# Kernel optimization log

Measured on AMD Instinct MI355X. Metric: run time of the kernel, lower is better.

## Reference

```python
import jax, jax.numpy as jnp
import numpy as np
from jax import lax

DIM = 192
HID = DIM // 2  # ffn_expansion_factor = 0.5 hardcoded in CFIM
B, H, W = 8, 160, 160
LAMBDA_C = 0.5
LAMBDA_S = 0.5


def _dwconv(x, w, dil):
    # depthwise 3x3 conv, NCHW, weight (C,1,3,3), 'same' padding with dilation
    return lax.conv_general_dilated(
        x, w, window_strides=(1, 1), padding=((dil, dil), (dil, dil)),
        rhs_dilation=(dil, dil), feature_group_count=w.shape[0],
        dimension_numbers=('NCHW', 'OIHW', 'NCHW'))


def setup_inputs() -> dict:
    key = jax.random.key(0)
    ks = jax.random.split(key, 12)
    s = 0.02
    return {
        'x1': jax.random.normal(ks[0], (B, DIM, H, W), jnp.float32),
        'x2': jax.random.normal(ks[1], (B, DIM, H, W), jnp.float32),
        # ChannelWeights MLP (reduction=1): Linear(4d,4d) -> ReLU -> Linear(4d,2d) -> Sigmoid
        'mlp_w1': jax.random.normal(ks[2], (4 * DIM, 4 * DIM), jnp.float32) * s,
        'mlp_b1': jnp.zeros((4 * DIM,), jnp.float32),
        'mlp_w2': jax.random.normal(ks[3], (2 * DIM, 4 * DIM), jnp.float32) * s,
        'mlp_b2': jnp.zeros((2 * DIM,), jnp.float32),
        # SpatialWeights: pointwise project_in (no bias), 3 depthwise 3x3, pointwise project_out
        'w_in': jax.random.normal(ks[4], (3 * HID, 2 * DIM), jnp.float32) * s,
        'w_dw1': jax.random.normal(ks[5], (HID, 1, 3, 3), jnp.float32) * s,  # center depth slice of the (3,3,3) kernel; padded-zero depth slices contribute nothing
        'w_dw2': jax.random.normal(ks[6], (HID, 1, 3, 3), jnp.float32) * s,
        'w_dw3': jax.random.normal(ks[7], (HID, 1, 3, 3), jnp.float32) * s,
        'w_out': jax.random.normal(ks[8], (2 * DIM, HID), jnp.float32) * s,
    }


def reference(x1, x2, mlp_w1, mlp_b1, mlp_w2, mlp_b2,
              w_in, w_dw1, w_dw2, w_dw3, w_out):
    b = x1.shape[0]
    dim = x1.shape[1]
    x = jnp.concatenate([x1, x2], axis=1)  # (B, 2*dim, H, W)

    # --- ChannelWeights ---
    avg = jnp.mean(x, axis=(2, 3))          # (B, 2*dim)
    mx = jnp.max(x, axis=(2, 3))            # (B, 2*dim)
    y = jnp.concatenate([avg, mx], axis=1)  # (B, 4*dim)
    y = jax.nn.relu(y @ mlp_w1.T + mlp_b1)
    y = jax.nn.sigmoid(y @ mlp_w2.T + mlp_b2)  # (B, 2*dim)
    cw = y.reshape(b, 2, dim, 1, 1)
    cw0, cw1 = cw[:, 0], cw[:, 1]           # each (B, dim, 1, 1)

    # --- SpatialWeights ---
    p = jnp.einsum('bchw,oc->bohw', x, w_in)  # 1x1 'Conv3d' project_in
    a, g2, g3 = jnp.split(p, 3, axis=1)       # each (B, HID, H, W)
    a = _dwconv(a, w_dw1, 1)
    g2 = _dwconv(g2, w_dw2, 2)
    g3 = _dwconv(g3, w_dw3, 3)
    g = jax.nn.gelu(a, approximate=False) * (g2 + g3)
    sw = jnp.einsum('bchw,oc->bohw', g, w_out)  # (B, 2*dim, H, W)
    sw0, sw1 = jnp.split(sw, 2, axis=1)

    # --- combine ---
    out_x1 = x1 + LAMBDA_C * cw1 * x2 + LAMBDA_S * sw1
    out_x2 = x2 + LAMBDA_C * cw0 * x1 + LAMBDA_S * sw0
    return (out_x1, out_x2)
```

## Files before the change

kernel.cpp:

```cpp
#include <hip/hip_runtime.h>
#include <cstdint>

#define HW 25600
#define WIDTH 160
#define NB 8
#define DIM 192
#define CH2 384
#define PCH 288
#define HID 96
#define PROW 176
#define PPS 29216
#define OUTN 39321600

typedef short bf16x8 __attribute__((ext_vector_type(8)));
typedef float f32x4 __attribute__((ext_vector_type(4)));

__device__ __forceinline__ unsigned short f2bf(float f) {
  union { float f; unsigned int u; } v; v.f = f;
  unsigned int u = v.u;
  u += 0x7FFFu + ((u >> 16) & 1u);
  return (unsigned short)(u >> 16);
}
__device__ __forceinline__ float bf2f(unsigned int bits16) {
  union { unsigned int u; float f; } v; v.u = bits16 << 16;
  return v.f;
}

__global__ void k_prep(const float* __restrict__ w, unsigned short* __restrict__ wa) {
  int i = blockIdx.x * 256 + threadIdx.x;
  float4 v = *(const float4*)(w + (size_t)i * 4);
  unsigned int lo = (unsigned int)f2bf(v.x) | ((unsigned int)f2bf(v.y) << 16);
  unsigned int hi = (unsigned int)f2bf(v.z) | ((unsigned int)f2bf(v.w) << 16);
  *(uint2*)(wa + (size_t)i * 4) = make_uint2(lo, hi);
}

__global__ void k_padzero(unsigned short* __restrict__ p) {
  unsigned short* base = p + (size_t)blockIdx.x * PPS;
  for (int i = threadIdx.x; i < 3616; i += 256) {
    int row, col;
    if (i < 1056) {
      int r = i / PROW; col = i - r * PROW;
      row = (r < 3) ? r : 160 + r;
    } else {
      int j = i - 1056;
      int r = j >> 4, cc = j & 15;
      row = 3 + r;
      col = (cc < 8) ? cc : 160 + cc;
    }
    base[row * PROW + col] = 0;
  }
}

__global__ void k_mlp1(const float* __restrict__ redsum, const float* __restrict__ redmax,
                       const float* __restrict__ w1, const float* __restrict__ b1,
                       float* __restrict__ h1) {
  int b = blockIdx.y;
  __shared__ float ybuf[768];
  int tid = threadIdx.x;
  for (int i = tid; i < 768; i += 256)
    ybuf[i] = (i < CH2) ? redsum[b * CH2 + i] * (1.0f / 25600.0f)
                        : redmax[b * CH2 + i - CH2];
  __syncthreads();
  int lane = tid & 63, wid = tid >> 6;
  int o0 = blockIdx.x * 256 + wid * 64;
  for (int oi = 0; oi < 64; ++oi) {
    int o = o0 + oi;
    const float* wr = w1 + (size_t)o * 768 + lane;
    float a = 0.f;
    #pragma unroll
    for (int j = 0; j < 12; ++j) a += wr[j * 64] * ybuf[lane + j * 64];
    #pragma unroll
    for (int k = 32; k >= 1; k >>= 1) a += __shfl_xor(a, k, 64);
    if (lane == 0) h1[b * 768 + o] = fmaxf(a + b1[o], 0.f);
  }
}

__global__ void k_mlp2(const float* __restrict__ h1, const float* __restrict__ w2,
                       const float* __restrict__ b2, float* __restrict__ cw) {
  int b = blockIdx.y;
  __shared__ float hbuf[768];
  int tid = threadIdx.x;
  for (int i = tid; i < 768; i += 256) hbuf[i] = h1[b * 768 + i];
  __syncthreads();
  int lane = tid & 63, wid = tid >> 6;
  int o0 = blockIdx.x * 256 + wid * 64;
  for (int oi = 0; oi < 64; ++oi) {
    int o = o0 + oi;
    if (o >= CH2) break;
    const float* wr = w2 + (size_t)o * 768 + lane;
    float a = 0.f;
    #pragma unroll
    for (int j = 0; j < 12; ++j) a += wr[j * 64] * hbuf[lane + j * 64];
    #pragma unroll
    for (int k = 32; k >= 1; k >>= 1) a += __shfl_xor(a, k, 64);
    if (lane == 0) cw[b * CH2 + o] = 1.f / (1.f + expf(-(a + b2[o])));
  }
}

#define G1_ST 72
__global__ __launch_bounds__(256, 2)
void k_gemm1(const float* __restrict__ x1, const float* __restrict__ x2,
             const unsigned short* __restrict__ wa, unsigned short* __restrict__ p,
             float* __restrict__ partial) {
  __shared__ short Blds[2][128 * G1_ST];
  __shared__ float psum[CH2];
  __shared__ float pmax[CH2];
  int tid = threadIdx.x;
  int bx = blockIdx.x, mz = blockIdx.y, b = blockIdx.z;
  int ns = bx * 128;
  int lane = tid & 63, wid = tid >> 6;
  int quad = lane >> 4, l15 = lane & 15;
  int wn = wid;
  int sg = tid & 31, cg0 = tid >> 5;
  int s4 = sg << 2;

  f32x4 acc[9][2];
  #pragma unroll
  for (int i = 0; i < 9; ++i) {
    acc[i][0] = (f32x4){0.f, 0.f, 0.f, 0.f};
    acc[i][1] = (f32x4){0.f, 0.f, 0.f, 0.f};
  }

  float4 R[8];

#define ISSUE_B(KK) do { \
    int kc_ = (KK) * 64; \
    const float* xb_ = (kc_ < DIM) ? (x1 + ((size_t)b * DIM + kc_) * HW) \
                                   : (x2 + ((size_t)b * DIM + (kc_ - DIM)) * HW); \
    _Pragma("unroll") \
    for (int it = 0; it < 2; ++it) { \
      const float* src_ = xb_ + (size_t)((cg0 + it * 8) << 2) * HW + ns + s4; \
      R[it * 4 + 0] = *(const float4*)(src_); \
      R[it * 4 + 1] = *(const float4*)(src_ + HW); \
      R[it * 4 + 2] = *(const float4*)(src_ + 2 * HW); \
      R[it * 4 + 3] = *(const float4*)(src_ + 3 * HW); \
    } \
  } while (0)

#define CONVERT_B(KK, BI) do { \
    int kc_ = (KK) * 64; \
    _Pragma("unroll") \
    for (int it = 0; it < 2; ++it) { \
      int c4_ = (cg0 + it * 8) << 2; \
      float4 r0 = R[it * 4 + 0], r1 = R[it * 4 + 1], r2 = R[it * 4 + 2], r3 = R[it * 4 + 3]; \
      unsigned short t0[4] = {f2bf(r0.x), f2bf(r0.y), f2bf(r0.z), f2bf(r0.w)}; \
      unsigned short t1[4] = {f2bf(r1.x), f2bf(r1.y), f2bf(r1.z), f2bf(r1.w)}; \
      unsigned short t2[4] = {f2bf(r2.x), f2bf(r2.y), f2bf(r2.z), f2bf(r2.w)}; \
      unsigned short t3[4] = {f2bf(r3.x), f2bf(r3.y), f2bf(r3.z), f2bf(r3.w)}; \
      _Pragma("unroll") \
      for (int j = 0; j < 4; ++j) { \
        unsigned int lo = (unsigned int)t0[j] | ((unsigned int)t1[j] << 16); \
        unsigned int hi = (unsigned int)t2[j] | ((unsigned int)t3[j] << 16); \
        *(uint2*)&Blds[BI][(s4 + j) * G1_ST + c4_] = make_uint2(lo, hi); \
      } \
      if (mz == 0) { \
        float s0 = r0.x + r0.y + r0.z + r0.w; \
        float s1 = r1.x + r1.y + r1.z + r1.w; \
        float s2 = r2.x + r2.y + r2.z + r2.w; \
        float s3 = r3.x + r3.y + r3.z + r3.w; \
        float m0 = fmaxf(fmaxf(r0.x, r0.y), fmaxf(r0.z, r0.w)); \
        float m1 = fmaxf(fmaxf(r1.x, r1.y), fmaxf(r1.z, r1.w)); \
        float m2 = fmaxf(fmaxf(r2.x, r2.y), fmaxf(r2.z, r2.w)); \
        float m3 = fmaxf(fmaxf(r3.x, r3.y), fmaxf(r3.z, r3.w)); \
        _Pragma("unroll") \
        for (int msk = 16; msk >= 1; msk >>= 1) { \
          s0 += __shfl_xor(s0, msk, 64); \
          s1 += __shfl_xor(s1, msk, 64); \
          s2 += __shfl_xor(s2, msk, 64); \
          s3 += __shfl_xor(s3, msk, 64); \
          m0 = fmaxf(m0, __shfl_xor(m0, msk, 64)); \
          m1 = fmaxf(m1, __shfl_xor(m1, msk, 64)); \
          m2 = fmaxf(m2, __shfl_xor(m2, msk, 64)); \
          m3 = fmaxf(m3, __shfl_xor(m3, msk, 64)); \
        } \
        if ((tid & 31) == 0) { \
          int ch_ = kc_ + c4_; \
          psum[ch_ + 0] = s0; psum[ch_ + 1] = s1; psum[ch_ + 2] = s2; psum[ch_ + 3] = s3; \
          pmax[ch_ + 0] = m0; pmax[ch_ + 1] = m1; pmax[ch_ + 2] = m2; pmax[ch_ + 3] = m3; \
        } \
      } \
    } \
  } while (0)

#define DO_MFMA(KK, BI) do { \
    const unsigned short* wab_ = wa + (size_t)(mz * 144 + l15) * CH2 + (KK) * 64 + quad * 8; \
    _Pragma("unroll") \
    for (int ks = 0; ks < 2; ++ks) { \
      int kof_ = ks * 32 + quad * 8; \
      bf16x8 b0_ = *(const bf16x8*)&Blds[BI][(wn * 32 + l15) * G1_ST + kof_]; \
      bf16x8 b1_ = *(const bf16x8*)&Blds[BI][(wn * 32 + 16 + l15) * G1_ST + kof_]; \
      _Pragma("unroll") \
      for (int mt = 0; mt < 9; ++mt) { \
        bf16x8 af_ = *(const bf16x8*)(wab_ + (size_t)mt * (16 * CH2) + ks * 32); \
        acc[mt][0] = __builtin_amdgcn_mfma_f32_16x16x32_bf16(af_, b0_, acc[mt][0], 0, 0, 0); \
        acc[mt][1] = __builtin_amdgcn_mfma_f32_16x16x32_bf16(af_, b1_, acc[mt][1], 0, 0, 0); \
      } \
    } \
  } while (0)

  ISSUE_B(0);
  CONVERT_B(0, 0);
  ISSUE_B(1);
  __syncthreads();
  #pragma unroll
  for (int kk = 0; kk < 6; ++kk) {
    DO_MFMA(kk, kk & 1);
    if (kk < 5) {
      CONVERT_B(kk + 1, (kk + 1) & 1);
      if (kk < 4) ISSUE_B(kk + 2);
      __syncthreads();
    }
  }

#undef ISSUE_B
#undef CONVERT_B
#undef DO_MFMA

  unsigned short* pb = p + (size_t)b * PCH * PPS;
  #pragma unroll
  for (int mt = 0; mt < 9; ++mt) {
    int obase = mz * 144 + mt * 16 + quad * 4;
    #pragma unroll
    for (int nt = 0; nt < 2; ++nt) {
      int s = ns + wn * 32 + nt * 16 + l15;
      int yy = s / WIDTH;
      int xx = s - yy * WIDTH;
      #pragma unroll
      for (int r = 0; r < 4; ++r) {
        int o = obase + r;
        pb[(size_t)o * PPS + (size_t)(yy + 3) * PROW + xx + 8] = f2bf(acc[mt][nt][r]);
      }
    }
  }

  if (mz == 0) {
    float* pp = partial + ((size_t)bx * 8 + b) * 768;
    for (int i = tid; i < 384; i += 256) {
      pp[i] = psum[i];
      pp[384 + i] = pmax[i];
    }
  }
}

__global__ void k_reduce(const float* __restrict__ partial, float* __restrict__ redsum,
                         float* __restrict__ redmax) {
  int col = blockIdx.x * 256 + threadIdx.x;
  int b = col / 768, j = col - b * 768;
  const float* src = partial + col;
  bool isSum = (j < 384);
  float a0, a1, a2, a3;
  if (isSum) { a0 = a1 = a2 = a3 = 0.f; }
  else       { a0 = a1 = a2 = a3 = -3.402823466e38f; }
  #pragma unroll 2
  for (int i = 0; i < 200; i += 4) {
    float v0 = src[(size_t)(i + 0) * 6144];
    float v1 = src[(size_t)(i + 1) * 6144];
    float v2 = src[(size_t)(i + 2) * 6144];
    float v3 = src[(size_t)(i + 3) * 6144];
    if (isSum) { a0 += v0; a1 += v1; a2 += v2; a3 += v3; }
    else { a0 = fmaxf(a0, v0); a1 = fmaxf(a1, v1); a2 = fmaxf(a2, v2); a3 = fmaxf(a3, v3); }
  }
  if (isSum) redsum[b * CH2 + j] = (a0 + a1) + (a2 + a3);
  else       redmax[b * CH2 + (j - 384)] = fmaxf(fmaxf(a0, a1), fmaxf(a2, a3));
}

#define TH 16
__global__ __launch_bounds__(256)
void k_dwgelu(const unsigned short* __restrict__ p,
              const float* __restrict__ wd1, const float* __restrict__ wd2,
              const float* __restrict__ wd3, unsigned short* __restrict__ g) {
  __shared__ unsigned lds[(18 + 20 + 22) * 88];
  unsigned* la = lds;
  unsigned* l2 = lds + 18 * 88;
  unsigned* l3 = lds + 38 * 88;

  int rg = blockIdx.x, c = blockIdx.y, b = blockIdx.z;
  int y0 = rg * TH;
  int tid = threadIdx.x;

  const unsigned short* pa = p + ((size_t)(b * PCH) + c) * PPS;
  const unsigned* srcA = (const unsigned*)(pa + (size_t)(y0 + 2) * PROW);
  const unsigned* src2 = (const unsigned*)(pa + (size_t)96 * PPS + (size_t)(y0 + 1) * PROW);
  const unsigned* src3 = (const unsigned*)(pa + (size_t)192 * PPS + (size_t)y0 * PROW);
  for (int i = tid; i < 18 * 88; i += 256) la[i] = srcA[i];
  for (int i = tid; i < 20 * 88; i += 256) l2[i] = src2[i];
  for (int i = tid; i < 22 * 88; i += 256) l3[i] = src3[i];

  float w1r[9], w2r[9], w3r[9];
  #pragma unroll
  for (int i = 0; i < 9; ++i) { w1r[i] = wd1[c * 9 + i]; w2r[i] = wd2[c * 9 + i]; w3r[i] = wd3[c * 9 + i]; }
  __syncthreads();

  int oy = tid >> 4;
  int cg = tid & 15;
  int ox0 = cg * 10;
  int ub = 3 + (ox0 >> 1);
  int ub3 = 2 + (ox0 >> 1);

  float acc_a[10], acc_g[10];
  #pragma unroll
  for (int i = 0; i < 10; ++i) { acc_a[i] = 0.f; acc_g[i] = 0.f; }

  #pragma unroll
  for (int ky = 0; ky < 3; ++ky) {
    const unsigned* rp = la + (oy + ky) * 88 + ub;
    float v[14];
    #pragma unroll
    for (int u = 0; u < 7; ++u) { unsigned d = rp[u]; v[2 * u] = bf2f(d & 0xFFFFu); v[2 * u + 1] = bf2f(d >> 16); }
    #pragma unroll
    for (int kx = 0; kx < 3; ++kx) {
      float wv = w1r[ky * 3 + kx];
      #pragma unroll
      for (int i = 0; i < 10; ++i) acc_a[i] += wv * v[i + kx + 1];
    }
  }
  #pragma unroll
  for (int ky = 0; ky < 3; ++ky) {
    const unsigned* rp = l2 + (oy + 2 * ky) * 88 + ub;
    float v[14];
    #pragma unroll
    for (int u = 0; u < 7; ++u) { unsigned d = rp[u]; v[2 * u] = bf2f(d & 0xFFFFu); v[2 * u + 1] = bf2f(d >> 16); }
    #pragma unroll
    for (int kx = 0; kx < 3; ++kx) {
      float wv = w2r[ky * 3 + kx];
      #pragma unroll
      for (int i = 0; i < 10; ++i) acc_g[i] += wv * v[i + 2 * kx];
    }
  }
  #pragma unroll
  for (int ky = 0; ky < 3; ++ky) {
    const unsigned* rp = l3 + (oy + 3 * ky) * 88 + ub3;
    float v[18];
    #pragma unroll
    for (int u = 0; u < 9; ++u) { unsigned d = rp[u]; v[2 * u] = bf2f(d & 0xFFFFu); v[2 * u + 1] = bf2f(d >> 16); }
    #pragma unroll
    for (int kx = 0; kx < 3; ++kx) {
      float wv = w3r[ky * 3 + kx];
      #pragma unroll
      for (int i = 0; i < 10; ++i) acc_g[i] += wv * v[i + 3 * kx + 1];
    }
  }

  unsigned short* gp = g + ((size_t)(b * HID) + c) * HW + (size_t)(y0 + oy) * WIDTH + ox0;
  #pragma unroll
  for (int j = 0; j < 5; ++j) {
    float a0 = acc_a[2 * j], a1 = acc_a[2 * j + 1];
    float g0 = 0.5f * a0 * (1.f + erff(a0 * 0.70710678118f)) * acc_g[2 * j];
    float g1 = 0.5f * a1 * (1.f + erff(a1 * 0.70710678118f)) * acc_g[2 * j + 1];
    ((unsigned*)gp)[j] = (unsigned)f2bf(g0) | ((unsigned)f2bf(g1) << 16);
  }
}

#define G2_ST 104
__global__ __launch_bounds__(256, 2)
void k_gemm2(const unsigned short* __restrict__ g, const float* __restrict__ w_out,
             const float* __restrict__ x1, const float* __restrict__ x2,
             const float* __restrict__ cw, float* __restrict__ out) {
  __shared__ short Alds[128 * G2_ST];
  __shared__ short Blds[128 * G2_ST];
  int tid = threadIdx.x;
  int ns = blockIdx.x * 128;
  int mo = blockIdx.y * 128;
  int b = blockIdx.z;
  int lane = tid & 63, wid = tid >> 6;
  int quad = lane >> 4, l15 = lane & 15;
  int wm = wid >> 1, wn = wid & 1;

  #pragma unroll
  for (int i = 0; i < 12; ++i) {
    int idx = i * 256 + tid;
    int row = idx / 24, c4 = (idx % 24) * 4;
    float4 w4 = *(const float4*)(w_out + (size_t)(mo + row) * HID + c4);
    unsigned int lo = (unsigned int)f2bf(w4.x) | ((unsigned int)f2bf(w4.y) << 16);
    unsigned int hi = (unsigned int)f2bf(w4.z) | ((unsigned int)f2bf(w4.w) << 16);
    *(uint2*)&Alds[row * G2_ST + c4] = make_uint2(lo, hi);
  }
  const unsigned short* gb = g + (size_t)b * HID * HW;
  #pragma unroll
  for (int it = 0; it < 3; ++it) {
    int idx = it * 256 + tid;
    int sg = idx & 31, cg = idx >> 5;
    int c4 = cg * 4, s4 = sg * 4;
    const unsigned short* src = gb + (size_t)c4 * HW + ns + s4;
    uint2 r0 = *(const uint2*)(src);
    uint2 r1 = *(const uint2*)(src + HW);
    uint2 r2 = *(const uint2*)(src + 2 * HW);
    uint2 r3 = *(const uint2*)(src + 3 * HW);
    unsigned short e0[4] = {(unsigned short)r0.x, (unsigned short)(r0.x >> 16), (unsigned short)r0.y, (unsigned short)(r0.y >> 16)};
    unsigned short e1[4] = {(unsigned short)r1.x, (unsigned short)(r1.x >> 16), (unsigned short)r1.y, (unsigned short)(r1.y >> 16)};
    unsigned short e2[4] = {(unsigned short)r2.x, (unsigned short)(r2.x >> 16), (unsigned short)r2.y, (unsigned short)(r2.y >> 16)};
    unsigned short e3[4] = {(unsigned short)r3.x, (unsigned short)(r3.x >> 16), (unsigned short)r3.y, (unsigned short)(r3.y >> 16)};
    #pragma unroll
    for (int j = 0; j < 4; ++j) {
      unsigned int lo = (unsigned int)e0[j] | ((unsigned int)e1[j] << 16);
      unsigned int hi = (unsigned int)e2[j] | ((unsigned int)e3[j] << 16);
      *(uint2*)&Blds[(s4 + j) * G2_ST + c4] = make_uint2(lo, hi);
    }
  }
  __syncthreads();

  f32x4 acc[4][4];
  #pragma unroll
  for (int i = 0; i < 4; ++i) {
    #pragma unroll
    for (int j = 0; j < 4; ++j) acc[i][j] = (f32x4){0.f, 0.f, 0.f, 0.f};
  }
  #pragma unroll
  for (int ks = 0; ks < 3; ++ks) {
    int kof = ks * 32 + quad * 8;
    bf16x8 bfr[4];
    #pragma unroll
    for (int nt = 0; nt < 4; ++nt)
      bfr[nt] = *(const bf16x8*)&Blds[(wn * 64 + nt * 16 + l15) * G2_ST + kof];
    #pragma unroll
    for (int mt = 0; mt < 4; ++mt) {
      bf16x8 af = *(const bf16x8*)&Alds[(wm * 64 + mt * 16 + l15) * G2_ST + kof];
      #pragma unroll
      for (int nt = 0; nt < 4; ++nt)
        acc[mt][nt] = __builtin_amdgcn_mfma_f32_16x16x32_bf16(af, bfr[nt], acc[mt][nt], 0, 0, 0);
    }
  }

  const float* cwb = cw + b * CH2;
  #pragma unroll
  for (int mt = 0; mt < 4; ++mt) {
    int o2b = mo + wm * 64 + mt * 16 + quad * 4;
    #pragma unroll
    for (int nt = 0; nt < 4; ++nt) {
      int s = ns + wn * 64 + nt * 16 + l15;
      #pragma unroll
      for (int r = 0; r < 4; ++r) {
        int o2 = o2b + r;
        int cch = (o2 < DIM) ? o2 : (o2 - DIM);
        size_t coff = ((size_t)b * DIM + cch) * HW + s;
        float v1 = x1[coff], v2 = x2[coff];
        float cwv = cwb[o2];
        float swv = acc[mt][nt][r];
        if (o2 < DIM) {
          out[OUTN + coff] = v2 + 0.5f * cwv * v1 + 0.5f * swv;
        } else {
          out[coff] = v1 + 0.5f * cwv * v2 + 0.5f * swv;
        }
      }
    }
  }
}

extern "C" void kernel_launch(void* const* d_in, const int* in_sizes, int n_in,
                              void* d_out, int out_size, void* d_ws, size_t ws_size,
                              hipStream_t stream) {
  const float* x1 = (const float*)d_in[0];
  const float* x2 = (const float*)d_in[1];
  const float* mlp_w1 = (const float*)d_in[2];
  const float* mlp_b1 = (const float*)d_in[3];
  const float* mlp_w2 = (const float*)d_in[4];
  const float* mlp_b2 = (const float*)d_in[5];
  const float* w_in = (const float*)d_in[6];
  const float* w_dw1 = (const float*)d_in[7];
  const float* w_dw2 = (const float*)d_in[8];
  const float* w_dw3 = (const float*)d_in[9];
  const float* w_out = (const float*)d_in[10];
  float* out = (float*)d_out;

  char* ws = (char*)d_ws;
  float* redsum       = (float*)(ws + 0);
  float* redmax       = (float*)(ws + 12288);
  float* h1           = (float*)(ws + 24576);
  float* cw           = (float*)(ws + 49152);
  unsigned short* p = (unsigned short*)(ws + 65536);
  char* gbase = ws + 65536 + 134627328;
  unsigned short* g = (unsigned short*)gbase;
  float* partial      = (float*)gbase;
  unsigned short* wA  = (unsigned short*)(gbase + 8388608);

  k_prep   <<<dim3(108),         dim3(256), 0, stream>>>(w_in, wA);
  k_padzero<<<dim3(2304),        dim3(256), 0, stream>>>(p);
  k_gemm1  <<<dim3(200, 2, 8),   dim3(256), 0, stream>>>(x1, x2, wA, p, partial);
  k_reduce <<<dim3(24),          dim3(256), 0, stream>>>(partial, redsum, redmax);
  k_mlp1   <<<dim3(3, 8),        dim3(256), 0, stream>>>(redsum, redmax, mlp_w1, mlp_b1, h1);
  k_mlp2   <<<dim3(2, 8),        dim3(256), 0, stream>>>(h1, mlp_w2, mlp_b2, cw);
  k_dwgelu <<<dim3(10, 96, 8),   dim3(256), 0, stream>>>(p, w_dw1, w_dw2, w_dw3, g);
  k_gemm2  <<<dim3(200, 3, 8),   dim3(256), 0, stream>>>(g, w_out, x1, x2, cw, out);
}
```

Before: 1.210 ms.

## Restructure output GEMM so each block pairs low/high channels and reads prepped bf16 weights

Weights for the output projection are converted to bf16 once by a new prep kernel writing into the (now dead) p buffer, and the GEMM reads A fragments directly from global memory instead of staging them in LDS. Each block now computes 64 channels for both output halves (c and c+DIM), so x1/x2 values at each position are loaded once and used for both outputs. The grid is reordered so the three channel blocks sharing a spatial tile run adjacently, and launch bounds request higher occupancy. This halves redundant x1/x2 reads and cuts LDS use, at the cost of uncached-LDS global weight loads per MFMA step.

```diff
diff --git a/kernel.cpp b/kernel.cpp
--- a/kernel.cpp
+++ b/kernel.cpp
@@ -32,6 +32,14 @@
   unsigned int lo = (unsigned int)f2bf(v.x) | ((unsigned int)f2bf(v.y) << 16);
   unsigned int hi = (unsigned int)f2bf(v.z) | ((unsigned int)f2bf(v.w) << 16);
   *(uint2*)(wa + (size_t)i * 4) = make_uint2(lo, hi);
+}
+
+__global__ void k_prep2(const float* __restrict__ w, unsigned short* __restrict__ wo) {
+  int i = blockIdx.x * 256 + threadIdx.x;
+  float4 v = *(const float4*)(w + (size_t)i * 4);
+  unsigned int lo = (unsigned int)f2bf(v.x) | ((unsigned int)f2bf(v.y) << 16);
+  unsigned int hi = (unsigned int)f2bf(v.z) | ((unsigned int)f2bf(v.w) << 16);
+  *(uint2*)(wo + (size_t)i * 4) = make_uint2(lo, hi);
 }
 
 __global__ void k_padzero(unsigned short* __restrict__ p) {
@@ -352,29 +360,19 @@
 }
 
 #define G2_ST 104
-__global__ __launch_bounds__(256, 2)
-void k_gemm2(const unsigned short* __restrict__ g, const float* __restrict__ w_out,
+__global__ __launch_bounds__(256, 4)
+void k_gemm2(const unsigned short* __restrict__ g, const unsigned short* __restrict__ wo,
              const float* __restrict__ x1, const float* __restrict__ x2,
              const float* __restrict__ cw, float* __restrict__ out) {
-  __shared__ short Alds[128 * G2_ST];
   __shared__ short Blds[128 * G2_ST];
   int tid = threadIdx.x;
-  int ns = blockIdx.x * 128;
-  int mo = blockIdx.y * 128;
+  int mo = blockIdx.x * 64;
+  int ns = blockIdx.y * 128;
   int b = blockIdx.z;
   int lane = tid & 63, wid = tid >> 6;
   int quad = lane >> 4, l15 = lane & 15;
-  int wm = wid >> 1, wn = wid & 1;
-
-  #pragma unroll
-  for (int i = 0; i < 12; ++i) {
-    int idx = i * 256 + tid;
-    int row = idx / 24, c4 = (idx % 24) * 4;
-    float4 w4 = *(const float4*)(w_out + (size_t)(mo + row) * HID + c4);
-    unsigned int lo = (unsigned int)f2bf(w4.x) | ((unsigned int)f2bf(w4.y) << 16);
-    unsigned int hi = (unsigned int)f2bf(w4.z) | ((unsigned int)f2bf(w4.w) << 16);
-    *(uint2*)&Alds[row * G2_ST + c4] = make_uint2(lo, hi);
-  }
+  int wn = wid;
+
   const unsigned short* gb = g + (size_t)b * HID * HW;
   #pragma unroll
   for (int it = 0; it < 3; ++it) {
@@ -399,48 +397,47 @@
   }
   __syncthreads();
 
-  f32x4 acc[4][4];
+  f32x4 accL[4][2], accH[4][2];
   #pragma unroll
   for (int i = 0; i < 4; ++i) {
     #pragma unroll
-    for (int j = 0; j < 4; ++j) acc[i][j] = (f32x4){0.f, 0.f, 0.f, 0.f};
+    for (int j = 0; j < 2; ++j) {
+      accL[i][j] = (f32x4){0.f, 0.f, 0.f, 0.f};
+      accH[i][j] = (f32x4){0.f, 0.f, 0.f, 0.f};
+    }
   }
   #pragma unroll
   for (int ks = 0; ks < 3; ++ks) {
     int kof = ks * 32 + quad * 8;
-    bf16x8 bfr[4];
-    #pragma unroll
-    for (int nt = 0; nt < 4; ++nt)
-      bfr[nt] = *(const bf16x8*)&Blds[(wn * 64 + nt * 16 + l15) * G2_ST + kof];
+    bf16x8 b0 = *(const bf16x8*)&Blds[(wn * 32 + l15) * G2_ST + kof];
+    bf16x8 b1 = *(const bf16x8*)&Blds[(wn * 32 + 16 + l15) * G2_ST + kof];
     #pragma unroll
     for (int mt = 0; mt < 4; ++mt) {
-      bf16x8 af = *(const bf16x8*)&Alds[(wm * 64 + mt * 16 + l15) * G2_ST + kof];
+      const unsigned short* wr = wo + (size_t)(mo + mt * 16 + l15) * HID + kof;
+      bf16x8 aL = *(const bf16x8*)(wr);
+      bf16x8 aH = *(const bf16x8*)(wr + (size_t)DIM * HID);
+      accL[mt][0] = __builtin_amdgcn_mfma_f32_16x16x32_bf16(aL, b0, accL[mt][0], 0, 0, 0);
+      accL[mt][1] = __builtin_amdgcn_mfma_f32_16x16x32_bf16(aL, b1, accL[mt][1], 0, 0, 0);
+      accH[mt][0] = __builtin_amdgcn_mfma_f32_16x16x32_bf16(aH, b0, accH[mt][0], 0, 0, 0);
+      accH[mt][1] = __builtin_amdgcn_mfma_f32_16x16x32_bf16(aH, b1, accH[mt][1], 0, 0, 0);
+    }
+  }
+
+  const float* cwb = cw + b * CH2;
+  #pragma unroll
+  for (int mt = 0; mt < 4; ++mt) {
+    #pragma unroll
+    for (int r = 0; r < 4; ++r) {
+      int c = mo + mt * 16 + quad * 4 + r;
+      float cw0v = cwb[c];
+      float cw1v = cwb[c + DIM];
       #pragma unroll
-      for (int nt = 0; nt < 4; ++nt)
-        acc[mt][nt] = __builtin_amdgcn_mfma_f32_16x16x32_bf16(af, bfr[nt], acc[mt][nt], 0, 0, 0);
-    }
-  }
-
-  const float* cwb = cw + b * CH2;
-  #pragma unroll
-  for (int mt = 0; mt < 4; ++mt) {
-    int o2b = mo + wm * 64 + mt * 16 + quad * 4;
-    #pragma unroll
-    for (int nt = 0; nt < 4; ++nt) {
-      int s = ns + wn * 64 + nt * 16 + l15;
-      #pragma unroll
-      for (int r = 0; r < 4; ++r) {
-        int o2 = o2b + r;
-        int cch = (o2 < DIM) ? o2 : (o2 - DIM);
-        size_t coff = ((size_t)b * DIM + cch) * HW + s;
+      for (int nt = 0; nt < 2; ++nt) {
+        int s = ns + wn * 32 + nt * 16 + l15;
+        size_t coff = ((size_t)b * DIM + c) * HW + s;
         float v1 = x1[coff], v2 = x2[coff];
-        float cwv = cwb[o2];
-        float swv = acc[mt][nt][r];
-        if (o2 < DIM) {
-          out[OUTN + coff] = v2 + 0.5f * cwv * v1 + 0.5f * swv;
-        } else {
-          out[coff] = v1 + 0.5f * cwv * v2 + 0.5f * swv;
-        }
+        out[OUTN + coff] = v2 + 0.5f * cw0v * v1 + 0.5f * accL[mt][nt][r];
+        out[coff]        = v1 + 0.5f * cw1v * v2 + 0.5f * accH[mt][nt][r];
       }
     }
   }
@@ -472,6 +469,7 @@
   unsigned short* g = (unsigned short*)gbase;
   float* partial      = (float*)gbase;
   unsigned short* wA  = (unsigned short*)(gbase + 8388608);
+  unsigned short* wOut = (unsigned short*)(ws + 65536);
 
   k_prep   <<<dim3(108),         dim3(256), 0, stream>>>(w_in, wA);
   k_padzero<<<dim3(2304),        dim3(256), 0, stream>>>(p);
@@ -480,5 +478,6 @@
   k_mlp1   <<<dim3(3, 8),        dim3(256), 0, stream>>>(redsum, redmax, mlp_w1, mlp_b1, h1);
   k_mlp2   <<<dim3(2, 8),        dim3(256), 0, stream>>>(h1, mlp_w2, mlp_b2, cw);
   k_dwgelu <<<dim3(10, 96, 8),   dim3(256), 0, stream>>>(p, w_dw1, w_dw2, w_dw3, g);
-  k_gemm2  <<<dim3(200, 3, 8),   dim3(256), 0, stream>>>(g, w_out, x1, x2, cw, out);
-}
+  k_prep2  <<<dim3(36),          dim3(256), 0, stream>>>(w_out, wOut);
+  k_gemm2  <<<dim3(3, 200, 8),   dim3(256), 0, stream>>>(g, wOut, x1, x2, cw, out);
+}
```

Result: faster. 1.089 ms (-10.0%).
